# Kernel optimization log

Hardware: AMD Instinct MI355X
Metric: run time of the kernel (lower is better)

The kernel has to match this reference:

```python
import jax, jax.numpy as jnp
import numpy as np

N = 50000       # nodes
E = 800000      # edges
F_IN = 128      # dataset.num_node_features
H = 128         # hidden_channels (all equal), pool_dim
FC1, FC2 = 512, 256
G = 512         # number of graphs
C = 32          # dataset.num_classes
EPS = 1e-5      # BatchNorm eps


def setup_inputs() -> dict:
    key = jax.random.key(0)
    ks = jax.random.split(key, 16)
    rn = lambda k, s: jax.random.normal(k, s, jnp.float32) * 0.05
    return {
        "x": jax.random.normal(ks[0], (N, F_IN), jnp.float32),
        "edge_index": jax.random.randint(ks[1], (2, E), 0, N),
        "batch": jnp.sort(jax.random.randint(ks[2], (N,), 0, G)),
        "W1": rn(ks[3], (F_IN, H)), "b1": jnp.zeros((H,), jnp.float32),
        "W2": rn(ks[4], (H, H)),    "b2": jnp.zeros((H,), jnp.float32),
        "W3": rn(ks[5], (H, H)),    "b3": jnp.zeros((H,), jnp.float32),
        "W4": rn(ks[6], (H, H)),    "b4": jnp.zeros((H,), jnp.float32),
        "lw1": rn(ks[7], (H, FC1)),   "lb1": jnp.zeros((FC1,), jnp.float32),
        "lw2": rn(ks[8], (FC1, FC2)), "lb2": jnp.zeros((FC2,), jnp.float32),
        "lw3": rn(ks[9], (FC2, C)),   "lb3": jnp.zeros((C,), jnp.float32),
        "g1": jnp.ones((FC1,), jnp.float32), "be1": jnp.zeros((FC1,), jnp.float32),
        "g2": jnp.ones((FC2,), jnp.float32), "be2": jnp.zeros((FC2,), jnp.float32),
    }


def _gcn_structure(edge_index):
    # add self loops, then symmetric deg^-1/2 normalization (PyG GCNConv default)
    loop = jnp.arange(N)
    src = jnp.concatenate([edge_index[0], loop])
    dst = jnp.concatenate([edge_index[1], loop])
    deg = jax.ops.segment_sum(jnp.ones_like(src, jnp.float32), dst, num_segments=N)
    dinv = jnp.where(deg > 0, jax.lax.rsqrt(deg), 0.0)
    norm = dinv[src] * dinv[dst]          # [E + N]
    return src, dst, norm


def _gcn_conv(x, src, dst, norm, W, b):
    h = x @ W                              # [N, out]
    agg = jax.ops.segment_sum(h[src] * norm[:, None], dst, num_segments=N)
    return agg + b


def _bn(h, gamma, beta):
    # training-mode batch stats (biased variance), as torch BatchNorm1d
    m = jnp.mean(h, axis=0)
    v = jnp.var(h, axis=0)
    return (h - m) * jax.lax.rsqrt(v + EPS) * gamma + beta


def reference(x, edge_index, batch, W1, b1, W2, b2, W3, b3, W4, b4,
              lw1, lb1, lw2, lb2, lw3, lb3, g1, be1, g2, be2):
    src, dst, norm = _gcn_structure(edge_index)
    x = jax.nn.relu(_gcn_conv(x, src, dst, norm, W1, b1))
    x = jax.nn.relu(_gcn_conv(x, src, dst, norm, W2, b2))
    x = jax.nn.relu(_gcn_conv(x, src, dst, norm, W3, b3))
    x = jax.nn.relu(_gcn_conv(x, src, dst, norm, W4, b4))
    # global_add_pool over graphs
    p = jax.ops.segment_sum(x, batch, num_segments=G)   # [G, H]
    h = jax.nn.relu(p @ lw1 + lb1)
    h = _bn(h, g1, be1)                                  # dropout = identity (eval)
    h = jax.nn.relu(h @ lw2 + lb2)
    h = _bn(h, g2, be2)
    return jax.nn.sigmoid(h @ lw3 + lb3)                 # [G, C]
```

## Files before the change

kernel.cpp:

```cpp
#include <hip/hip_runtime.h>
#include <hip/hip_fp16.h>
#include <math.h>

#define NN 50000
#define NE 800000
#define FT 128
#define NG 512
#define F1 512
#define F2 256
#define NC 32
#define BN_EPS 1e-5f

typedef __attribute__((ext_vector_type(8))) unsigned short ushort8;
typedef __attribute__((ext_vector_type(8))) _Float16 f16x8;
typedef __attribute__((ext_vector_type(4))) float f32x4;

__device__ __forceinline__ unsigned short f2h(float f) {
  return __half_as_ushort(__float2half(f));
}
__device__ __forceinline__ float h2f(unsigned short h) {
  return __half2float(__ushort_as_half(h));
}


__global__ __launch_bounds__(256) void k_hist(const int* __restrict__ ei, int* __restrict__ cnt) {
  int e = blockIdx.x * 256 + threadIdx.x;
  if (e < NE) atomicAdd(&cnt[ei[NE + e]], 1);
}

__global__ __launch_bounds__(256) void k_dinv(const int* __restrict__ cnt, float* __restrict__ dinv) {
  int i = blockIdx.x * 256 + threadIdx.x;
  if (i < NN) dinv[i] = rsqrtf((float)(cnt[i] + 1));
}

__global__ __launch_bounds__(256) void k_scan1(const int* __restrict__ cnt, int* __restrict__ bsum) {
  __shared__ int s[256];
  int t = threadIdx.x, i = blockIdx.x * 256 + t;
  s[t] = (i < NN) ? cnt[i] : 0;
  __syncthreads();
  for (int d = 128; d > 0; d >>= 1) {
    if (t < d) s[t] += s[t + d];
    __syncthreads();
  }
  if (t == 0) bsum[blockIdx.x] = s[0];
}

__global__ __launch_bounds__(256) void k_scan2(const int* __restrict__ bsum, int* __restrict__ bscan, int nb) {
  __shared__ int s[256];
  int t = threadIdx.x;
  int v = (t < nb) ? bsum[t] : 0;
  s[t] = v; __syncthreads();
  for (int d = 1; d < 256; d <<= 1) {
    int a = (t >= d) ? s[t - d] : 0;
    __syncthreads();
    s[t] += a;
    __syncthreads();
  }
  bscan[t] = s[t] - v;
}

__global__ __launch_bounds__(256) void k_scan3(const int* __restrict__ cnt, const int* __restrict__ bscan,
                                               int* __restrict__ off) {
  __shared__ int s[256];
  int t = threadIdx.x, i = blockIdx.x * 256 + t;
  int v = (i < NN) ? cnt[i] : 0;
  s[t] = v; __syncthreads();
  for (int d = 1; d < 256; d <<= 1) {
    int a = (t >= d) ? s[t - d] : 0;
    __syncthreads();
    s[t] += a;
    __syncthreads();
  }
  int base = bscan[blockIdx.x];
  if (i < NN) off[i] = base + s[t] - v;
  if (i == NN - 1) off[NN] = base + s[t];
}

__global__ __launch_bounds__(256) void k_fill(const int* __restrict__ ei, const int* __restrict__ off,
                                              int* __restrict__ cur, const float* __restrict__ dinv,
                                              unsigned int* __restrict__ ep) {
  int e = blockIdx.x * 256 + threadIdx.x;
  if (e >= NE) return;
  int s = ei[e], d = ei[NE + e];
  int p = off[d] + atomicAdd(&cur[d], 1);
  float w = dinv[s] * dinv[d];
  ep[p] = (unsigned int)(s & 0xFFFF) | ((unsigned int)f2h(w) << 16);
}


__global__ __launch_bounds__(256) void k_wprep(const float* __restrict__ W, unsigned short* __restrict__ Wt) {
  int idx = blockIdx.x * 256 + threadIdx.x;
  int c = idx >> 7, k = idx & 127;
  int byte = c * 256 + k * 2;
  byte ^= (c & 7) << 4;
  Wt[byte >> 1] = f2h(W[k * FT + c]);
}


template <int FIRST>
__global__ __launch_bounds__(256) void k_gemm_mfma(const float* __restrict__ Xf,
                                                   const unsigned short* __restrict__ Xh,
                                                   const unsigned short* __restrict__ Wt,
                                                   unsigned short* __restrict__ Oc) {
  __shared__ unsigned short sA[64 * 128];
  __shared__ unsigned short sB[128 * 128];
  int t = threadIdx.x;
#pragma unroll
  for (int i = 0; i < 8; ++i) {
    int off = t * 16 + i * 4096;
    *(float4*)((char*)sB + off) = *(const float4*)((const char*)Wt + off);
  }
  {
    int row = t >> 2, k0 = (t & 3) * 32;
    int grow = blockIdx.x * 64 + row;
    if (grow >= NN) grow = NN - 1;
    if (FIRST) {
      const float* xr = Xf + (size_t)grow * FT + k0;
#pragma unroll
      for (int j = 0; j < 4; ++j) {
        float4 v0 = *(const float4*)&xr[j * 8];
        float4 v1 = *(const float4*)&xr[j * 8 + 4];
        ushort8 w;
        w[0] = f2h(v0.x); w[1] = f2h(v0.y); w[2] = f2h(v0.z); w[3] = f2h(v0.w);
        w[4] = f2h(v1.x); w[5] = f2h(v1.y); w[6] = f2h(v1.z); w[7] = f2h(v1.w);
        int byte = row * 256 + (k0 + j * 8) * 2;
        byte ^= (row & 7) << 4;
        *(ushort8*)((char*)sA + byte) = w;
      }
    } else {
#pragma unroll
      for (int j = 0; j < 4; ++j) {
        int k = k0 + j * 8;
        int ch = k >> 4, wo = k & 15;
        ushort8 v = *(const ushort8*)&Xh[((size_t)ch * NN + grow) * 16 + wo];
        int byte = row * 256 + k * 2;
        byte ^= (row & 7) << 4;
        *(ushort8*)((char*)sA + byte) = v;
      }
    }
  }
  __syncthreads();
  int w = t >> 6, l = t & 63;
  int m = l & 15, ks = l >> 4;
  f16x8 a[4];
#pragma unroll
  for (int kk = 0; kk < 4; ++kk) {
    int r = w * 16 + m;
    int byte = r * 256 + (kk * 32 + ks * 8) * 2;
    byte ^= (r & 7) << 4;
    a[kk] = *(const f16x8*)((const char*)sA + byte);
  }
  f32x4 acc[8];
#pragma unroll
  for (int nf = 0; nf < 8; ++nf) acc[nf] = (f32x4){0.f, 0.f, 0.f, 0.f};
#pragma unroll
  for (int nf = 0; nf < 8; ++nf) {
#pragma unroll
    for (int kk = 0; kk < 4; ++kk) {
      int col = nf * 16 + m;
      int byte = col * 256 + (kk * 32 + ks * 8) * 2;
      byte ^= (col & 7) << 4;
      f16x8 b = *(const f16x8*)((const char*)sB + byte);
      acc[nf] = __builtin_amdgcn_mfma_f32_16x16x32_f16(a[kk], b, acc[nf], 0, 0, 0);
    }
  }
  int orow0 = blockIdx.x * 64 + w * 16 + ks * 4;
#pragma unroll
  for (int nf = 0; nf < 8; ++nf) {
#pragma unroll
    for (int r = 0; r < 4; ++r) {
      int orow = orow0 + r;
      if (orow < NN) Oc[((size_t)nf * NN + orow) * 16 + m] = f2h(acc[nf][r]);
    }
  }
}


__global__ __launch_bounds__(256) void k_aggc(const unsigned short* __restrict__ Hc,
                                              const float* __restrict__ dinv,
                                              const int* __restrict__ off, const unsigned int* __restrict__ ep,
                                              const float* __restrict__ bias, unsigned short* __restrict__ O) {
  int c = blockIdx.x & 7;
  int grp = blockIdx.x >> 3;
  int t = threadIdx.x;
  int node = grp * 128 + (t >> 1);
  int half = t & 1;
  if (node >= NN) return;
  const unsigned short* base = Hc + (size_t)c * NN * 16 + half * 8;
  float di = dinv[node];
  float sw = di * di;
  float acc[8];
  {
    ushort8 sv = *(const ushort8*)&base[(size_t)node * 16];
#pragma unroll
    for (int i = 0; i < 8; ++i) acc[i] = h2f(sv[i]) * sw;
  }
  int e0 = off[node], e1 = off[node + 1];
  int e = e0;
  for (; e + 4 <= e1; e += 4) {
    unsigned int p0 = ep[e], p1 = ep[e + 1], p2 = ep[e + 2], p3 = ep[e + 3];
    ushort8 v0 = *(const ushort8*)&base[(size_t)(p0 & 0xFFFFu) * 16];
    ushort8 v1 = *(const ushort8*)&base[(size_t)(p1 & 0xFFFFu) * 16];
    ushort8 v2 = *(const ushort8*)&base[(size_t)(p2 & 0xFFFFu) * 16];
    ushort8 v3 = *(const ushort8*)&base[(size_t)(p3 & 0xFFFFu) * 16];
    float w0 = h2f((unsigned short)(p0 >> 16));
    float w1 = h2f((unsigned short)(p1 >> 16));
    float w2 = h2f((unsigned short)(p2 >> 16));
    float w3 = h2f((unsigned short)(p3 >> 16));
#pragma unroll
    for (int i = 0; i < 8; ++i) acc[i] += h2f(v0[i]) * w0;
#pragma unroll
    for (int i = 0; i < 8; ++i) acc[i] += h2f(v1[i]) * w1;
#pragma unroll
    for (int i = 0; i < 8; ++i) acc[i] += h2f(v2[i]) * w2;
#pragma unroll
    for (int i = 0; i < 8; ++i) acc[i] += h2f(v3[i]) * w3;
  }
  for (; e < e1; ++e) {
    unsigned int pv = ep[e];
    float w = h2f((unsigned short)(pv >> 16));
    ushort8 v = *(const ushort8*)&base[(size_t)(pv & 0xFFFFu) * 16];
#pragma unroll
    for (int i = 0; i < 8; ++i) acc[i] += h2f(v[i]) * w;
  }
  ushort8 outv;
#pragma unroll
  for (int i = 0; i < 8; ++i) {
    float v = acc[i] + bias[c * 16 + half * 8 + i];
    outv[i] = f2h(fmaxf(v, 0.f));
  }
  *(ushort8*)&O[((size_t)c * NN + node) * 16 + half * 8] = outv;
}


__global__ __launch_bounds__(256) void k_bounds(const int* __restrict__ batch, int* __restrict__ gstart,
                                                int* __restrict__ gend) {
  int i = blockIdx.x * 256 + threadIdx.x;
  if (i >= NN) return;
  int b = batch[i];
  if (i == 0 || batch[i - 1] != b) gstart[b] = i;
  if (i == NN - 1 || batch[i + 1] != b) gend[b] = i + 1;
}

__global__ __launch_bounds__(128) void k_pool(const unsigned short* __restrict__ X, const int* __restrict__ gstart,
                                              const int* __restrict__ gend, float* __restrict__ pool) {
  int g = blockIdx.x, t = threadIdx.x;
  int ch = t >> 4, wo = t & 15;
  float s = 0.f;
  int n0 = gstart[g], n1 = gend[g];
  const unsigned short* base = X + (size_t)ch * NN * 16 + wo;
  for (int n = n0; n < n1; ++n) s += h2f(base[(size_t)n * 16]);
  pool[g * FT + t] = s;
}


__global__ __launch_bounds__(256) void k_fc1(const float* __restrict__ P, const float* __restrict__ W,
                                             const float* __restrict__ B, float* __restrict__ O) {
  __shared__ float sp[FT];
  int g = blockIdx.x, t = threadIdx.x;
  if (t < FT) sp[t] = P[g * FT + t];
  __syncthreads();
  float a0 = B[t], a1 = B[t + 256];
  for (int k = 0; k < FT; ++k) {
    float x = sp[k];
    a0 += x * W[k * F1 + t];
    a1 += x * W[k * F1 + t + 256];
  }
  O[g * F1 + t] = fmaxf(a0, 0.f);
  O[g * F1 + t + 256] = fmaxf(a1, 0.f);
}

__global__ __launch_bounds__(256) void k_bnstats(const float* __restrict__ h, int cols,
                                                 float* __restrict__ bm, float* __restrict__ br) {
  __shared__ float ss[256], s2[256];
  int c = blockIdx.x, t = threadIdx.x;
  float a = 0.f, b = 0.f;
  for (int r = t; r < NG; r += 256) {
    float v = h[r * cols + c];
    a += v; b += v * v;
  }
  ss[t] = a; s2[t] = b; __syncthreads();
  for (int d = 128; d > 0; d >>= 1) {
    if (t < d) { ss[t] += ss[t + d]; s2[t] += s2[t + d]; }
    __syncthreads();
  }
  if (t == 0) {
    float m = ss[0] / NG;
    float var = s2[0] / NG - m * m;
    bm[c] = m;
    br[c] = rsqrtf(var + BN_EPS);
  }
}

__global__ __launch_bounds__(256) void k_fc2(const float* __restrict__ H1, const float* __restrict__ bm,
                                             const float* __restrict__ br, const float* __restrict__ gam,
                                             const float* __restrict__ bet, const float* __restrict__ W,
                                             const float* __restrict__ B, float* __restrict__ O) {
  __shared__ float sh[F1];
  int g = blockIdx.x, t = threadIdx.x;
  for (int k = t; k < F1; k += 256) {
    float v = H1[g * F1 + k];
    sh[k] = (v - bm[k]) * br[k] * gam[k] + bet[k];
  }
  __syncthreads();
  float a = B[t];
  for (int k = 0; k < F1; ++k) a += sh[k] * W[k * F2 + t];
  O[g * F2 + t] = fmaxf(a, 0.f);
}

__global__ __launch_bounds__(256) void k_fc3(const float* __restrict__ H2, const float* __restrict__ bm,
                                             const float* __restrict__ br, const float* __restrict__ gam,
                                             const float* __restrict__ bet, const float* __restrict__ W,
                                             const float* __restrict__ B, float* __restrict__ O) {
  __shared__ float sh[F2];
  int g = blockIdx.x, t = threadIdx.x;
  if (t < F2) {
    float v = H2[g * F2 + t];
    sh[t] = (v - bm[t]) * br[t] * gam[t] + bet[t];
  }
  __syncthreads();
  if (t < NC) {
    float a = B[t];
    for (int k = 0; k < F2; ++k) a += sh[k] * W[k * NC + t];
    O[g * NC + t] = 1.f / (1.f + expf(-a));
  }
}


extern "C" void kernel_launch(void* const* d_in, const int* in_sizes, int n_in,
                              void* d_out, int out_size, void* d_ws, size_t ws_size,
                              hipStream_t stream) {
  const float* x     = (const float*)d_in[0];
  const int*   ei    = (const int*)d_in[1];
  const int*   batch = (const int*)d_in[2];
  const float* Wc[4] = {(const float*)d_in[3], (const float*)d_in[5], (const float*)d_in[7], (const float*)d_in[9]};
  const float* Bc[4] = {(const float*)d_in[4], (const float*)d_in[6], (const float*)d_in[8], (const float*)d_in[10]};
  const float* lw1 = (const float*)d_in[11]; const float* lb1 = (const float*)d_in[12];
  const float* lw2 = (const float*)d_in[13]; const float* lb2 = (const float*)d_in[14];
  const float* lw3 = (const float*)d_in[15]; const float* lb3 = (const float*)d_in[16];
  const float* g1  = (const float*)d_in[17]; const float* be1 = (const float*)d_in[18];
  const float* g2  = (const float*)d_in[19]; const float* be2 = (const float*)d_in[20];

  char* p = (char*)d_ws;
  auto take = [&](size_t bytes) {
    char* r = p;
    p += (bytes + 255) & ~(size_t)255;
    return r;
  };
  int*   cnt    = (int*)take((size_t)NN * 4);
  float* dinv   = (float*)take((size_t)NN * 4);
  int*   off    = (int*)take((size_t)(NN + 1) * 4);
  int*   cur    = (int*)take((size_t)NN * 4);
  int*   bsum   = (int*)take(256 * 4);
  int*   bscan  = (int*)take(256 * 4);
  int*   gstart = (int*)take((size_t)NG * 4);
  int*   gend   = (int*)take((size_t)NG * 4);
  unsigned int*   ep   = (unsigned int*)take((size_t)NE * 4);
  unsigned short* Wt   = (unsigned short*)take((size_t)FT * FT * 2);
  unsigned short* bufT = (unsigned short*)take((size_t)NN * FT * 2);
  unsigned short* bufA = (unsigned short*)take((size_t)NN * FT * 2);
  unsigned short* bufB = (unsigned short*)take((size_t)NN * FT * 2);
  float* pool   = (float*)take((size_t)NG * FT * 4);
  float* h1     = (float*)take((size_t)NG * F1 * 4);
  float* h2     = (float*)take((size_t)NG * F2 * 4);
  float* bnm1   = (float*)take(F1 * 4);
  float* bnr1   = (float*)take(F1 * 4);
  float* bnm2   = (float*)take(F2 * 4);
  float* bnr2   = (float*)take(F2 * 4);

  const int NB = (NN + 255) / 256;

  hipMemsetAsync(cnt, 0, (size_t)NN * 4, stream);
  hipMemsetAsync(cur, 0, (size_t)NN * 4, stream);
  hipMemsetAsync(gstart, 0, (size_t)NG * 4, stream);
  hipMemsetAsync(gend, 0, (size_t)NG * 4, stream);

  k_hist<<<NE / 256, 256, 0, stream>>>(ei, cnt);
  k_dinv<<<NB, 256, 0, stream>>>(cnt, dinv);
  k_scan1<<<NB, 256, 0, stream>>>(cnt, bsum);
  k_scan2<<<1, 256, 0, stream>>>(bsum, bscan, NB);
  k_scan3<<<NB, 256, 0, stream>>>(cnt, bscan, off);
  k_fill<<<NE / 256, 256, 0, stream>>>(ei, off, cur, dinv, ep);

  const int NBLK_G = (NN + 63) / 64;
  const int NGRP_A = (NN + 127) / 128;
  unsigned short* outs[4] = {bufA, bufB, bufA, bufB};
  for (int l = 0; l < 4; ++l) {
    k_wprep<<<64, 256, 0, stream>>>(Wc[l], Wt);
    if (l == 0)
      k_gemm_mfma<1><<<NBLK_G, 256, 0, stream>>>(x, (const unsigned short*)nullptr, Wt, bufT);
    else
      k_gemm_mfma<0><<<NBLK_G, 256, 0, stream>>>((const float*)nullptr, outs[l - 1], Wt, bufT);
    k_aggc<<<NGRP_A * 8, 256, 0, stream>>>(bufT, dinv, off, ep, Bc[l], outs[l]);
  }

  k_bounds<<<NB, 256, 0, stream>>>(batch, gstart, gend);
  k_pool<<<NG, 128, 0, stream>>>(bufB, gstart, gend, pool);

  k_fc1<<<NG, 256, 0, stream>>>(pool, lw1, lb1, h1);
  k_bnstats<<<F1, 256, 0, stream>>>(h1, F1, bnm1, bnr1);
  k_fc2<<<NG, 256, 0, stream>>>(h1, bnm1, bnr1, g1, be1, lw2, lb2, h2);
  k_bnstats<<<F2, 256, 0, stream>>>(h2, F2, bnm2, bnr2);
  k_fc3<<<NG, 256, 0, stream>>>(h2, bnm2, bnr2, g2, be2, lw3, lb3, (float*)d_out);
}
```

Before: 374.9 us.

## Widen feature chunk layout to 32 channels and deepen gather unroll

Result: faster. 343.3 us (-8.4%).

```diff
diff --git a/kernel.cpp b/kernel.cpp
--- a/kernel.cpp
+++ b/kernel.cpp
@@ -131,8 +131,8 @@
 #pragma unroll
       for (int j = 0; j < 4; ++j) {
         int k = k0 + j * 8;
-        int ch = k >> 4, wo = k & 15;
-        ushort8 v = *(const ushort8*)&Xh[((size_t)ch * NN + grow) * 16 + wo];
+        int ch = k >> 5, ko = k & 31;
+        ushort8 v = *(const ushort8*)&Xh[((size_t)ch * NN + grow) * 32 + ko];
         int byte = row * 256 + k * 2;
         byte ^= (row & 7) << 4;
         *(ushort8*)((char*)sA + byte) = v;
@@ -167,10 +167,12 @@
   int orow0 = blockIdx.x * 64 + w * 16 + ks * 4;
 #pragma unroll
   for (int nf = 0; nf < 8; ++nf) {
+    int ch = nf >> 1;
+    int co = ((nf & 1) << 4) + m;
 #pragma unroll
     for (int r = 0; r < 4; ++r) {
       int orow = orow0 + r;
-      if (orow < NN) Oc[((size_t)nf * NN + orow) * 16 + m] = f2h(acc[nf][r]);
+      if (orow < NN) Oc[((size_t)ch * NN + orow) * 32 + co] = f2h(acc[nf][r]);
     }
   }
 }
@@ -180,29 +182,43 @@
                                               const float* __restrict__ dinv,
                                               const int* __restrict__ off, const unsigned int* __restrict__ ep,
                                               const float* __restrict__ bias, unsigned short* __restrict__ O) {
-  int c = blockIdx.x & 7;
-  int grp = blockIdx.x >> 3;
+  int c = blockIdx.x & 3;
+  int grp = blockIdx.x >> 2;
   int t = threadIdx.x;
-  int node = grp * 128 + (t >> 1);
-  int half = t & 1;
+  int node = grp * 64 + (t >> 2);
+  int l = t & 3;
   if (node >= NN) return;
-  const unsigned short* base = Hc + (size_t)c * NN * 16 + half * 8;
+  const unsigned short* base = Hc + (size_t)c * NN * 32 + l * 8;
   float di = dinv[node];
   float sw = di * di;
   float acc[8];
   {
-    ushort8 sv = *(const ushort8*)&base[(size_t)node * 16];
+    ushort8 sv = *(const ushort8*)&base[(size_t)node * 32];
 #pragma unroll
     for (int i = 0; i < 8; ++i) acc[i] = h2f(sv[i]) * sw;
   }
   int e0 = off[node], e1 = off[node + 1];
   int e = e0;
+  for (; e + 8 <= e1; e += 8) {
+    unsigned int pw[8];
+#pragma unroll
+    for (int j = 0; j < 8; ++j) pw[j] = ep[e + j];
+    ushort8 v[8];
+#pragma unroll
+    for (int j = 0; j < 8; ++j) v[j] = *(const ushort8*)&base[(size_t)(pw[j] & 0xFFFFu) * 32];
+#pragma unroll
+    for (int j = 0; j < 8; ++j) {
+      float w = h2f((unsigned short)(pw[j] >> 16));
+#pragma unroll
+      for (int i = 0; i < 8; ++i) acc[i] += h2f(v[j][i]) * w;
+    }
+  }
   for (; e + 4 <= e1; e += 4) {
     unsigned int p0 = ep[e], p1 = ep[e + 1], p2 = ep[e + 2], p3 = ep[e + 3];
-    ushort8 v0 = *(const ushort8*)&base[(size_t)(p0 & 0xFFFFu) * 16];
-    ushort8 v1 = *(const ushort8*)&base[(size_t)(p1 & 0xFFFFu) * 16];
-    ushort8 v2 = *(const ushort8*)&base[(size_t)(p2 & 0xFFFFu) * 16];
-    ushort8 v3 = *(const ushort8*)&base[(size_t)(p3 & 0xFFFFu) * 16];
+    ushort8 v0 = *(const ushort8*)&base[(size_t)(p0 & 0xFFFFu) * 32];
+    ushort8 v1 = *(const ushort8*)&base[(size_t)(p1 & 0xFFFFu) * 32];
+    ushort8 v2 = *(const ushort8*)&base[(size_t)(p2 & 0xFFFFu) * 32];
+    ushort8 v3 = *(const ushort8*)&base[(size_t)(p3 & 0xFFFFu) * 32];
     float w0 = h2f((unsigned short)(p0 >> 16));
     float w1 = h2f((unsigned short)(p1 >> 16));
     float w2 = h2f((unsigned short)(p2 >> 16));
@@ -219,17 +235,17 @@
   for (; e < e1; ++e) {
     unsigned int pv = ep[e];
     float w = h2f((unsigned short)(pv >> 16));
-    ushort8 v = *(const ushort8*)&base[(size_t)(pv & 0xFFFFu) * 16];
+    ushort8 v = *(const ushort8*)&base[(size_t)(pv & 0xFFFFu) * 32];
 #pragma unroll
     for (int i = 0; i < 8; ++i) acc[i] += h2f(v[i]) * w;
   }
   ushort8 outv;
 #pragma unroll
   for (int i = 0; i < 8; ++i) {
-    float v = acc[i] + bias[c * 16 + half * 8 + i];
+    float v = acc[i] + bias[c * 32 + l * 8 + i];
     outv[i] = f2h(fmaxf(v, 0.f));
   }
-  *(ushort8*)&O[((size_t)c * NN + node) * 16 + half * 8] = outv;
+  *(ushort8*)&O[((size_t)c * NN + node) * 32 + l * 8] = outv;
 }
 
 
@@ -245,11 +261,11 @@
 __global__ __launch_bounds__(128) void k_pool(const unsigned short* __restrict__ X, const int* __restrict__ gstart,
                                               const int* __restrict__ gend, float* __restrict__ pool) {
   int g = blockIdx.x, t = threadIdx.x;
-  int ch = t >> 4, wo = t & 15;
+  int ch = t >> 5, wo = t & 31;
   float s = 0.f;
   int n0 = gstart[g], n1 = gend[g];
-  const unsigned short* base = X + (size_t)ch * NN * 16 + wo;
-  for (int n = n0; n < n1; ++n) s += h2f(base[(size_t)n * 16]);
+  const unsigned short* base = X + (size_t)ch * NN * 32 + wo;
+  for (int n = n0; n < n1; ++n) s += h2f(base[(size_t)n * 32]);
   pool[g * FT + t] = s;
 }
 
@@ -383,7 +399,7 @@
   k_fill<<<NE / 256, 256, 0, stream>>>(ei, off, cur, dinv, ep);
 
   const int NBLK_G = (NN + 63) / 64;
-  const int NGRP_A = (NN + 127) / 128;
+  const int NGRP_A = (NN + 63) / 64;
   unsigned short* outs[4] = {bufA, bufB, bufA, bufB};
   for (int l = 0; l < 4; ++l) {
     k_wprep<<<64, 256, 0, stream>>>(Wc[l], Wt);
@@ -391,7 +407,7 @@
       k_gemm_mfma<1><<<NBLK_G, 256, 0, stream>>>(x, (const unsigned short*)nullptr, Wt, bufT);
     else
       k_gemm_mfma<0><<<NBLK_G, 256, 0, stream>>>((const float*)nullptr, outs[l - 1], Wt, bufT);
-    k_aggc<<<NGRP_A * 8, 256, 0, stream>>>(bufT, dinv, off, ep, Bc[l], outs[l]);
+    k_aggc<<<NGRP_A * 4, 256, 0, stream>>>(bufT, dinv, off, ep, Bc[l], outs[l]);
   }
 
   k_bounds<<<NB, 256, 0, stream>>>(batch, gstart, gend);
```
